# Kernel optimization log

Hardware: AMD Instinct MI355X
Metric: run time of the kernel (lower is better)

## Reference

```python
import jax, jax.numpy as jnp
import numpy as np

D_MODEL = 512
B, T = 4, 4096


def setup_inputs() -> dict:
    key = jax.random.key(0)
    k1, k2, k3 = jax.random.split(key, 3)
    x = jax.random.normal(k1, (B, T, D_MODEL), dtype=jnp.float32)
    # torch nn.Linear weight layout: [out_features, in_features]
    w_qkv = jax.random.normal(k2, (3 * D_MODEL, D_MODEL), dtype=jnp.float32) * (1.0 / np.sqrt(D_MODEL))
    w_proj = jax.random.normal(k3, (D_MODEL, D_MODEL), dtype=jnp.float32) * (1.0 / np.sqrt(D_MODEL))
    return {"x": x, "w_qkv": w_qkv, "w_proj": w_proj}


def reference(x, w_qkv, w_proj):
    # Faithful to the torch module: NO head split; attention over full d_model.
    Bx, Tx, C = x.shape
    qkv = jnp.einsum('btc,oc->bto', x, w_qkv)  # [B,T,3C]
    q, k, v = jnp.split(qkv, 3, axis=-1)
    scale = 1.0 / jnp.sqrt(jnp.asarray(C, x.dtype))
    scores = jnp.einsum('btc,bsc->bts', q, k) * scale  # [B,T,T]
    causal = jnp.tril(jnp.ones((Tx, Tx), dtype=bool))
    scores = jnp.where(causal[None, :, :], scores, -jnp.inf)
    weights = jax.nn.softmax(scores, axis=-1)
    out = jnp.einsum('bts,bsc->btc', weights, v)
    return jnp.einsum('btc,oc->bto', out, w_proj)
```

## Files before the change

kernel.cpp:

```cpp
#include <hip/hip_runtime.h>
#include <hip/hip_bf16.h>
#include <stdint.h>

typedef __bf16 bf16_t;
typedef __bf16 bf16x4 __attribute__((ext_vector_type(4)));
typedef __bf16 bf16x8 __attribute__((ext_vector_type(8)));
typedef short s16x4 __attribute__((ext_vector_type(4)));
typedef float f32x4 __attribute__((ext_vector_type(4)));

static_assert(sizeof(bf16x8) == 16, "bf16x8 must be 16B");

#define MFMA_BF16(a, b, c) __builtin_amdgcn_mfma_f32_16x16x32_bf16((a), (b), (c), 0, 0, 0)

__device__ __forceinline__ f32x4 mfma16(bf16x4 a, bf16x4 b, f32x4 c) {
#if __has_builtin(__builtin_amdgcn_mfma_f32_16x16x16bf16_1k)
  union { bf16x4 h; s16x4 s; } ua, ub;
  ua.h = a;
  ub.h = b;
  return __builtin_amdgcn_mfma_f32_16x16x16bf16_1k(ua.s, ub.s, c, 0, 0, 0);
#else
  f32x4 d = c;
  asm volatile("v_mfma_f32_16x16x16_bf16 %0, %1, %2, %0" : "+v"(d) : "v"(a), "v"(b));
  return d;
#endif
}

typedef const __attribute__((address_space(1))) void* gas_ptr;
typedef __attribute__((address_space(3))) void* las_ptr;

__device__ __forceinline__ void gload_lds16(const void* g, void* l) {
  __builtin_amdgcn_global_load_lds((gas_ptr)g, (las_ptr)l, 16, 0, 0);
}

#define NEG_BIG (-1.0e30f)

__global__ __launch_bounds__(256) void cvt_kernel(const float* __restrict__ src,
                                                  bf16_t* __restrict__ dst) {
  const int i = (blockIdx.x * 256 + threadIdx.x) * 4;
  const f32x4 v = *(const f32x4*)(src + i);
  bf16x4 o;
  o[0] = (bf16_t)v[0];
  o[1] = (bf16_t)v[1];
  o[2] = (bf16_t)v[2];
  o[3] = (bf16_t)v[3];
  *(bf16x4*)(dst + i) = o;
}

template <int MODE>
__global__ __launch_bounds__(256, 2) void gemm_bt_kernel(
    const bf16_t* __restrict__ A, const bf16_t* __restrict__ Bw,
    bf16_t* __restrict__ o_q, bf16_t* __restrict__ o_k, bf16_t* __restrict__ o_vT,
    float* __restrict__ o_f) {
  constexpr int K = 512;
  __shared__ bf16_t As[128 * 32];
  __shared__ bf16_t Bs[128 * 32];

  const int tid = threadIdx.x;
  const int lane = tid & 63;
  const int wid = tid >> 6;
  const int quad = lane >> 4;
  const int l15 = lane & 15;
  const int wm = wid >> 1;
  const int wn = wid & 1;

  const int mt = blockIdx.x & 127;
  const int nt = blockIdx.x >> 7;
  const int row0 = mt * 128;
  const int col0 = nt * 128;

  f32x4 acc[4][4] = {};

  for (int kt = 0; kt < K; kt += 32) {
    __syncthreads();
#pragma unroll
    for (int rnd = 0; rnd < 2; rnd++) {
      const int e = (rnd * 256 + tid) * 8;
      const int r = e >> 5;
      const int c = e & 31;
      gload_lds16(A + (size_t)(row0 + r) * K + kt + c, As + e);
      gload_lds16(Bw + (size_t)(col0 + r) * K + kt + c, Bs + e);
    }
    __syncthreads();

    bf16x8 af[4], bfr[4];
#pragma unroll
    for (int i = 0; i < 4; i++)
      af[i] = *(const bf16x8*)(As + (wm * 64 + i * 16 + l15) * 32 + quad * 8);
#pragma unroll
    for (int i = 0; i < 4; i++)
      bfr[i] = *(const bf16x8*)(Bs + (wn * 64 + i * 16 + l15) * 32 + quad * 8);
#pragma unroll
    for (int mi = 0; mi < 4; mi++)
#pragma unroll
      for (int ni = 0; ni < 4; ni++)
        acc[mi][ni] = MFMA_BF16(af[mi], bfr[ni], acc[mi][ni]);
  }

#pragma unroll
  for (int mi = 0; mi < 4; mi++) {
    const int row = row0 + wm * 64 + mi * 16 + quad * 4;
#pragma unroll
    for (int ni = 0; ni < 4; ni++) {
      const int col = col0 + wn * 64 + ni * 16 + l15;
#pragma unroll
      for (int r = 0; r < 4; r++) {
        const int rr = row + r;
        if constexpr (MODE == 0) {
          const bf16_t bv = (bf16_t)acc[mi][ni][r];
          if (col < 512) {
            o_q[(size_t)rr * 512 + col] = bv;
          } else if (col < 1024) {
            o_k[(size_t)rr * 512 + (col - 512)] = bv;
          } else {
            const int bb = rr >> 12;
            const int t = rr & 4095;
            o_vT[((size_t)bb * 512 + (col - 1024)) * 4096 + t] = bv;
          }
        } else {
          o_f[(size_t)rr * 512 + col] = acc[mi][ni][r];
        }
      }
    }
  }
}

__global__ __launch_bounds__(256, 2) void attn_part_kernel(
    const bf16_t* __restrict__ q, const bf16_t* __restrict__ k,
    const bf16_t* __restrict__ vT, bf16_t* __restrict__ partO,
    float2* __restrict__ stats) {
  __shared__ bf16_t SB[2][16384];

  const int tid = threadIdx.x;
  const int lane = tid & 63;
  const int wid = tid >> 6;
  const int quad = lane >> 4;
  const int l15 = lane & 15;

  const int bid = blockIdx.x;
  const int b = bid & 3;
  const int w = bid >> 2;
  int g = 0;
  while (w >= 4 * (g + 1) * (g + 2)) g++;
  const int rem = w - 4 * g * (g + 1);
  const int i = rem / (g + 1);
  const int c = rem - i * (g + 1);
  const int s = 8 * g + i;

  const int t0w = s * 64 + wid * 16;
  const int kv0 = c * 512;
  const int mmax = min(31, (t0w + 15 - kv0) >> 4);
  const int kvtmax = mmax >> 2;
  const int mmax_blk = min(31, (s * 64 + 63 - kv0) >> 4);
  const int kvtmax_blk = mmax_blk >> 2;

  const float scale = 0.044194173824159216f;
  const bf16_t* kbase = k + ((size_t)b * 4096 + kv0) * 512;
  const bf16_t* vbase = vT + ((size_t)b * 512) * 4096 + kv0;

  auto stageK = [&](int kt, int buf) {
    for (int rnd = 0; rnd <= kvtmax_blk; rnd++) {
      const int ch = rnd * 256 + tid;
      const int g4 = ch >> 4;
      const int w16 = ch & 15;
      const int cg = (w16 >> 2) ^ (g4 & 3);
      const int row = g4 * 4 + (w16 & 3);
      gload_lds16(kbase + (size_t)row * 512 + kt * 32 + cg * 8,
                  &SB[buf][ch * 8]);
    }
  };
  auto stageV = [&](int dh, int kvt, int buf) {
    const bf16_t* vb = vbase + (size_t)(dh * 256) * 4096;
#pragma unroll
    for (int rnd = 0; rnd < 8; rnd++) {
      const int ch = rnd * 256 + tid;
      const int d = ch >> 3;
      const int cg = (ch & 7) ^ (d & 7);
      gload_lds16(vb + (size_t)d * 4096 + kvt * 64 + cg * 8, &SB[buf][ch * 8]);
    }
  };

  stageK(0, 0);

  bf16x8 qf[16];
  {
    const bf16_t* qp = q + ((size_t)(b * 4096 + t0w + l15)) * 512 + quad * 8;
#pragma unroll
    for (int kk = 0; kk < 16; kk++) qf[kk] = *(const bf16x8*)(qp + kk * 32);
  }

  f32x4 Sacc[32];
#pragma unroll
  for (int m = 0; m < 32; m++) Sacc[m] = f32x4{0.f, 0.f, 0.f, 0.f};

  const int abase =
      ((l15 >> 2) * 16 + (quad ^ ((l15 >> 2) & 3)) * 4 + (l15 & 3)) * 8;

  __syncthreads();

  int cur = 0;
#pragma unroll
  for (int kt = 0; kt < 16; kt++) {
    if (kt < 15)
      stageK(kt + 1, cur ^ 1);
    else
      stageV(0, 0, cur ^ 1);

    const bf16_t* sb = &SB[cur][0];
    __builtin_amdgcn_s_setprio(1);
#pragma unroll
    for (int m = 0; m < 32; m++) {
      if (m <= mmax) {
        const bf16x8 kf = *(const bf16x8*)(sb + abase + m * 512);
        Sacc[m] = MFMA_BF16(kf, qf[kt], Sacc[m]);
      }
    }
    __builtin_amdgcn_s_setprio(0);
    __syncthreads();
    cur ^= 1;
  }

  const int qr = t0w + l15;
  float mx = NEG_BIG;
#pragma unroll
  for (int m = 0; m < 32; m++) {
    if (m <= mmax) {
#pragma unroll
      for (int r = 0; r < 4; r++) {
        const int kv = kv0 + m * 16 + quad * 4 + r;
        const float vvv = (kv <= qr) ? Sacc[m][r] : NEG_BIG;
        Sacc[m][r] = vvv;
        mx = fmaxf(mx, vvv);
      }
    }
  }
  mx = fmaxf(mx, __shfl_xor(mx, 16));
  mx = fmaxf(mx, __shfl_xor(mx, 32));

  float lrow = 0.0f;
  bf16x4 pb[32];
#pragma unroll
  for (int m = 0; m < 32; m++) {
    bf16x4 pv = {};
    if (m <= mmax) {
#pragma unroll
      for (int r = 0; r < 4; r++) {
        const float p = __expf((Sacc[m][r] - mx) * scale);
        pv[r] = (bf16_t)p;
        lrow += p;
      }
    }
    pb[m] = pv;
  }
  lrow += __shfl_xor(lrow, 16);
  lrow += __shfl_xor(lrow, 32);

  if (quad == 0)
    stats[((size_t)w * 4 + b) * 64 + wid * 16 + l15] =
        make_float2(mx * scale, lrow);

  const int l64 = l15 * 64;
  const int qh = quad >> 1;
  const int ql = (quad & 1) * 4;
  const int s7 = l15 & 7;

  for (int dh = 0; dh < 2; dh++) {
    f32x4 Oacc[16];
#pragma unroll
    for (int dt = 0; dt < 16; dt++) Oacc[dt] = f32x4{0.f, 0.f, 0.f, 0.f};

    for (int kvt = 0; kvt <= kvtmax_blk; kvt++) {
      if (kvt < kvtmax_blk)
        stageV(dh, kvt + 1, cur ^ 1);
      else if (dh == 0)
        stageV(1, 0, cur ^ 1);

      if (kvt <= kvtmax) {
        const bf16_t* sb = &SB[cur][0];
        __builtin_amdgcn_s_setprio(1);
#pragma unroll
        for (int dt = 0; dt < 16; dt++) {
#pragma unroll
          for (int gg = 0; gg < 4; gg++) {
            const bf16x4 vf = *(const bf16x4*)(
                sb + dt * 1024 + l64 + (((gg * 2 + qh) ^ s7) << 3) + ql);
            Oacc[dt] = mfma16(pb[kvt * 4 + gg], vf, Oacc[dt]);
          }
        }
        __builtin_amdgcn_s_setprio(0);
      }
      __syncthreads();
      cur ^= 1;
    }

    bf16_t* pbase = partO + (size_t)bid * 32768 + dh * 256;
#pragma unroll
    for (int rr = 0; rr < 4; rr++) {
      bf16_t* prow = pbase + (size_t)(wid * 16 + quad * 4 + rr) * 512 + l15;
#pragma unroll
      for (int dt = 0; dt < 16; dt++) prow[dt * 16] = (bf16_t)Oacc[dt][rr];
    }
  }
}

__global__ __launch_bounds__(256) void attn_combine_kernel(
    const bf16_t* __restrict__ partO, const float2* __restrict__ stats,
    bf16_t* __restrict__ o) {
  const int b = blockIdx.x & 3;
  const int s = blockIdx.x >> 2;
  const int g = s >> 3;
  const int nc = g + 1;
  const int w0 = 4 * g * (g + 1) + (s & 7) * (g + 1);

  __shared__ float wgt[8][64];
  __shared__ float linv[64];

  const int tid = threadIdx.x;
  if (tid < 64) {
    float mc[8], lc[8];
    float M = NEG_BIG;
    for (int cc = 0; cc < nc; cc++) {
      const float2 ml = stats[((size_t)(w0 + cc) * 4 + b) * 64 + tid];
      mc[cc] = ml.x;
      lc[cc] = ml.y;
      M = fmaxf(M, ml.x);
    }
    float L = 0.0f;
    for (int cc = 0; cc < nc; cc++) {
      const float wv = __expf(mc[cc] - M);
      wgt[cc][tid] = wv;
      L += wv * lc[cc];
    }
    linv[tid] = (L > 0.0f) ? 1.0f / L : 0.0f;
  }
  __syncthreads();

#pragma unroll
  for (int it = 0; it < 16; it++) {
    const int idx = it * 256 + tid;
    const int row = idx >> 6;
    const int d8 = (idx & 63) * 8;
    float acc[8] = {};
    for (int cc = 0; cc < nc; cc++) {
      const int bidc = ((w0 + cc) << 2) | b;
      const bf16x8 p = *(const bf16x8*)(partO + (size_t)bidc * 32768 +
                                        (size_t)row * 512 + d8);
      const float wv = wgt[cc][row];
#pragma unroll
      for (int e = 0; e < 8; e++) acc[e] += wv * (float)p[e];
    }
    const float li = linv[row];
    bf16x8 ov;
#pragma unroll
    for (int e = 0; e < 8; e++) ov[e] = (bf16_t)(acc[e] * li);
    *(bf16x8*)(o + ((size_t)(b * 4096 + s * 64 + row)) * 512 + d8) = ov;
  }
}

extern "C" void kernel_launch(void* const* d_in, const int* in_sizes, int n_in,
                              void* d_out, int out_size, void* d_ws, size_t ws_size,
                              hipStream_t stream) {
  const float* x_f = (const float*)d_in[0];
  const float* wq_f = (const float*)d_in[1];
  const float* wp_f = (const float*)d_in[2];
  float* out = (float*)d_out;

  bf16_t* xb = (bf16_t*)d_ws;
  bf16_t* wqb = xb + (size_t)16384 * 512;
  bf16_t* wpb = wqb + (size_t)1536 * 512;
  bf16_t* q = wpb + (size_t)512 * 512;
  bf16_t* kk = q + (size_t)16384 * 512;
  bf16_t* vT = kk + (size_t)16384 * 512;
  bf16_t* partO = vT + (size_t)16384 * 512;
  float2* stats = (float2*)(partO + (size_t)1152 * 32768);

  cvt_kernel<<<(16384 * 512) / 1024, 256, 0, stream>>>(x_f, xb);
  cvt_kernel<<<(1536 * 512) / 1024, 256, 0, stream>>>(wq_f, wqb);
  cvt_kernel<<<(512 * 512) / 1024, 256, 0, stream>>>(wp_f, wpb);

  gemm_bt_kernel<0><<<128 * 12, 256, 0, stream>>>(xb, wqb, q, kk, vT, nullptr);
  attn_part_kernel<<<1152, 256, 0, stream>>>(q, kk, vT, partO, stats);
  attn_combine_kernel<<<256, 256, 0, stream>>>(partO, stats, xb);
  gemm_bt_kernel<1><<<128 * 4, 256, 0, stream>>>(xb, wpb, nullptr, nullptr, nullptr, out);
}
```

Before: 422.1 us.

## Deepen attention load pipeline, change partial-O layout, merge conversion kernels

The attention-partial kernel now runs one unified slice stream over K and V tiles. It keeps two global-to-LDS loads in flight, gated by explicit vmcnt waits and raw barriers, where before a single prefetch sat behind __syncthreads. Partial outputs are written as contiguous bf16x4 per lane in a fragment-native layout, and the combine kernel reads that layout and transposes through swizzled LDS into coalesced row stores. The three fp32-to-bf16 conversion launches are merged into one. K staging now always issues 8 rounds even when fewer rows are needed, which adds some load traffic, and the hand-tuned waitcnt logic risks ordering bugs.

```diff
diff --git a/kernel.cpp b/kernel.cpp
--- a/kernel.cpp
+++ b/kernel.cpp
@@ -32,18 +32,32 @@
   __builtin_amdgcn_global_load_lds((gas_ptr)g, (las_ptr)l, 16, 0, 0);
 }
 
+#define ORDER_FENCE() asm volatile("" ::: "memory")
+
 #define NEG_BIG (-1.0e30f)
 
-__global__ __launch_bounds__(256) void cvt_kernel(const float* __restrict__ src,
-                                                  bf16_t* __restrict__ dst) {
+__global__ __launch_bounds__(256) void cvt3_kernel(
+    const float* __restrict__ x, const float* __restrict__ wq,
+    const float* __restrict__ wp, bf16_t* __restrict__ xb,
+    bf16_t* __restrict__ wqb, bf16_t* __restrict__ wpb) {
   const int i = (blockIdx.x * 256 + threadIdx.x) * 4;
-  const f32x4 v = *(const f32x4*)(src + i);
+  const float* src;
+  bf16_t* dst;
+  int off;
+  if (i < 8388608) {
+    src = x; dst = xb; off = 0;
+  } else if (i < 9175040) {
+    src = wq; dst = wqb; off = 8388608;
+  } else {
+    src = wp; dst = wpb; off = 9175040;
+  }
+  const f32x4 v = *(const f32x4*)(src + (i - off));
   bf16x4 o;
   o[0] = (bf16_t)v[0];
   o[1] = (bf16_t)v[1];
   o[2] = (bf16_t)v[2];
   o[3] = (bf16_t)v[3];
-  *(bf16x4*)(dst + i) = o;
+  *(bf16x4*)(dst + (i - off)) = o;
 }
 
 template <int MODE>
@@ -151,35 +165,44 @@
   const int mmax = min(31, (t0w + 15 - kv0) >> 4);
   const int kvtmax = mmax >> 2;
   const int mmax_blk = min(31, (s * 64 + 63 - kv0) >> 4);
-  const int kvtmax_blk = mmax_blk >> 2;
+  const int NV = (mmax_blk >> 2) + 1;
+  const int NSLICE = 16 + 2 * NV;
 
   const float scale = 0.044194173824159216f;
   const bf16_t* kbase = k + ((size_t)b * 4096 + kv0) * 512;
   const bf16_t* vbase = vT + ((size_t)b * 512) * 4096 + kv0;
 
-  auto stageK = [&](int kt, int buf) {
-    for (int rnd = 0; rnd <= kvtmax_blk; rnd++) {
-      const int ch = rnd * 256 + tid;
-      const int g4 = ch >> 4;
-      const int w16 = ch & 15;
-      const int cg = (w16 >> 2) ^ (g4 & 3);
-      const int row = g4 * 4 + (w16 & 3);
-      gload_lds16(kbase + (size_t)row * 512 + kt * 32 + cg * 8,
-                  &SB[buf][ch * 8]);
+  auto stage_slice = [&](int u, int buf) {
+    if (u < 16) {
+#pragma unroll
+      for (int rnd = 0; rnd < 8; rnd++) {
+        const int ch = rnd * 256 + tid;
+        const int g4 = ch >> 4;
+        const int w16 = ch & 15;
+        const int cg = (w16 >> 2) ^ (g4 & 3);
+        const int row = g4 * 4 + (w16 & 3);
+        gload_lds16(kbase + (size_t)row * 512 + u * 32 + cg * 8,
+                    &SB[buf][ch * 8]);
+      }
+    } else {
+      const int v = u - 16;
+      const int dh = (v >= NV) ? 1 : 0;
+      const int kvt = v - dh * NV;
+      const bf16_t* vb = vbase + (size_t)(dh * 256) * 4096;
+#pragma unroll
+      for (int rnd = 0; rnd < 8; rnd++) {
+        const int ch = rnd * 256 + tid;
+        const int d = ch >> 3;
+        const int cg = (ch & 7) ^ (d & 7);
+        gload_lds16(vb + (size_t)d * 4096 + kvt * 64 + cg * 8, &SB[buf][ch * 8]);
+      }
     }
   };
-  auto stageV = [&](int dh, int kvt, int buf) {
-    const bf16_t* vb = vbase + (size_t)(dh * 256) * 4096;
-#pragma unroll
-    for (int rnd = 0; rnd < 8; rnd++) {
-      const int ch = rnd * 256 + tid;
-      const int d = ch >> 3;
-      const int cg = (ch & 7) ^ (d & 7);
-      gload_lds16(vb + (size_t)d * 4096 + kvt * 64 + cg * 8, &SB[buf][ch * 8]);
-    }
-  };
-
-  stageK(0, 0);
+
+  stage_slice(0, 0);
+  ORDER_FENCE();
+  stage_slice(1, 1);
+  ORDER_FENCE();
 
   bf16x8 qf[16];
   {
@@ -195,16 +218,12 @@
   const int abase =
       ((l15 >> 2) * 16 + (quad ^ ((l15 >> 2) & 3)) * 4 + (l15 & 3)) * 8;
 
-  __syncthreads();
-
   int cur = 0;
 #pragma unroll
   for (int kt = 0; kt < 16; kt++) {
-    if (kt < 15)
-      stageK(kt + 1, cur ^ 1);
-    else
-      stageV(0, 0, cur ^ 1);
-
+    asm volatile("s_waitcnt vmcnt(8)" ::: "memory");
+    __builtin_amdgcn_sched_barrier(0);
+    __builtin_amdgcn_s_barrier();
     const bf16_t* sb = &SB[cur][0];
     __builtin_amdgcn_s_setprio(1);
 #pragma unroll
@@ -215,7 +234,10 @@
       }
     }
     __builtin_amdgcn_s_setprio(0);
-    __syncthreads();
+    asm volatile("s_waitcnt lgkmcnt(0)" ::: "memory");
+    __builtin_amdgcn_sched_barrier(0);
+    __builtin_amdgcn_s_barrier();
+    stage_slice(kt + 2, cur);
     cur ^= 1;
   }
 
@@ -263,41 +285,53 @@
   const int ql = (quad & 1) * 4;
   const int s7 = l15 & 7;
 
+#pragma unroll
   for (int dh = 0; dh < 2; dh++) {
     f32x4 Oacc[16];
 #pragma unroll
     for (int dt = 0; dt < 16; dt++) Oacc[dt] = f32x4{0.f, 0.f, 0.f, 0.f};
 
-    for (int kvt = 0; kvt <= kvtmax_blk; kvt++) {
-      if (kvt < kvtmax_blk)
-        stageV(dh, kvt + 1, cur ^ 1);
-      else if (dh == 0)
-        stageV(1, 0, cur ^ 1);
-
-      if (kvt <= kvtmax) {
-        const bf16_t* sb = &SB[cur][0];
-        __builtin_amdgcn_s_setprio(1);
-#pragma unroll
-        for (int dt = 0; dt < 16; dt++) {
-#pragma unroll
-          for (int gg = 0; gg < 4; gg++) {
-            const bf16x4 vf = *(const bf16x4*)(
-                sb + dt * 1024 + l64 + (((gg * 2 + qh) ^ s7) << 3) + ql);
-            Oacc[dt] = mfma16(pb[kvt * 4 + gg], vf, Oacc[dt]);
+#pragma unroll
+    for (int kvt = 0; kvt < 8; kvt++) {
+      if (kvt < NV) {
+        const int u = 16 + dh * NV + kvt;
+        if (u < NSLICE - 1)
+          asm volatile("s_waitcnt vmcnt(8)" ::: "memory");
+        else
+          asm volatile("s_waitcnt vmcnt(0)" ::: "memory");
+        __builtin_amdgcn_sched_barrier(0);
+        __builtin_amdgcn_s_barrier();
+        if (kvt <= kvtmax) {
+          const bf16_t* sb = &SB[cur][0];
+          __builtin_amdgcn_s_setprio(1);
+#pragma unroll
+          for (int dt = 0; dt < 16; dt++) {
+#pragma unroll
+            for (int gg = 0; gg < 4; gg++) {
+              const bf16x4 vf = *(const bf16x4*)(
+                  sb + dt * 1024 + l64 + (((gg * 2 + qh) ^ s7) << 3) + ql);
+              Oacc[dt] = mfma16(pb[kvt * 4 + gg], vf, Oacc[dt]);
+            }
+          }
+          __builtin_amdgcn_s_setprio(0);
+        }
+        if (kvt == NV - 1) {
+          bf16_t* pbase =
+              partO + (size_t)bid * 32768 + dh * 16384 + wid * 4096;
+#pragma unroll
+          for (int dt = 0; dt < 16; dt++) {
+            bf16x4 ov;
+#pragma unroll
+            for (int r = 0; r < 4; r++) ov[r] = (bf16_t)Oacc[dt][r];
+            *(bf16x4*)(pbase + dt * 256 + l15 * 16 + quad * 4) = ov;
           }
         }
-        __builtin_amdgcn_s_setprio(0);
-      }
-      __syncthreads();
-      cur ^= 1;
-    }
-
-    bf16_t* pbase = partO + (size_t)bid * 32768 + dh * 256;
-#pragma unroll
-    for (int rr = 0; rr < 4; rr++) {
-      bf16_t* prow = pbase + (size_t)(wid * 16 + quad * 4 + rr) * 512 + l15;
-#pragma unroll
-      for (int dt = 0; dt < 16; dt++) prow[dt * 16] = (bf16_t)Oacc[dt][rr];
+        asm volatile("s_waitcnt lgkmcnt(0)" ::: "memory");
+        __builtin_amdgcn_sched_barrier(0);
+        __builtin_amdgcn_s_barrier();
+        if (u + 2 < NSLICE) stage_slice(u + 2, cur);
+        cur ^= 1;
+      }
     }
   }
 }
@@ -313,6 +347,7 @@
 
   __shared__ float wgt[8][64];
   __shared__ float linv[64];
+  __shared__ bf16_t TB[64 * 256];
 
   const int tid = threadIdx.x;
   if (tid < 64) {
@@ -334,25 +369,46 @@
   }
   __syncthreads();
 
-#pragma unroll
-  for (int it = 0; it < 16; it++) {
-    const int idx = it * 256 + tid;
-    const int row = idx >> 6;
-    const int d8 = (idx & 63) * 8;
-    float acc[8] = {};
+  const int quad = tid & 3;
+  const int l15 = (tid >> 2) & 15;
+  const int wid = tid >> 6;
+  const int q0 = wid * 16 + quad * 4;
+  const f32x4 li4 = *(const f32x4*)(&linv[q0]);
+
+  for (int dh = 0; dh < 2; dh++) {
+    f32x4 acc4[16] = {};
     for (int cc = 0; cc < nc; cc++) {
-      const int bidc = ((w0 + cc) << 2) | b;
-      const bf16x8 p = *(const bf16x8*)(partO + (size_t)bidc * 32768 +
-                                        (size_t)row * 512 + d8);
-      const float wv = wgt[cc][row];
-#pragma unroll
-      for (int e = 0; e < 8; e++) acc[e] += wv * (float)p[e];
-    }
-    const float li = linv[row];
-    bf16x8 ov;
-#pragma unroll
-    for (int e = 0; e < 8; e++) ov[e] = (bf16_t)(acc[e] * li);
-    *(bf16x8*)(o + ((size_t)(b * 4096 + s * 64 + row)) * 512 + d8) = ov;
+      const bf16_t* pp = partO + (size_t)(((w0 + cc) << 2) | b) * 32768 +
+                         dh * 16384 + wid * 4096 + l15 * 16 + quad * 4;
+      const f32x4 wv4 = *(const f32x4*)(&wgt[cc][q0]);
+#pragma unroll
+      for (int dt = 0; dt < 16; dt++) {
+        const bf16x4 p = *(const bf16x4*)(pp + dt * 256);
+#pragma unroll
+        for (int e = 0; e < 4; e++) acc4[dt][e] += wv4[e] * (float)p[e];
+      }
+    }
+#pragma unroll
+    for (int dt = 0; dt < 16; dt++) {
+      const int d2 = (dt * 16 + l15) * 2;
+#pragma unroll
+      for (int r = 0; r < 4; r++) {
+        const int qq = q0 + r;
+        *(bf16_t*)((char*)TB + qq * 512 + (d2 ^ ((qq & 7) << 4))) =
+            (bf16_t)(acc4[dt][r] * li4[r]);
+      }
+    }
+    __syncthreads();
+    const int row = tid >> 2;
+    const int quarter = tid & 3;
+    bf16_t* orow =
+        o + ((size_t)(b * 4096 + s * 64 + row)) * 512 + dh * 256 + quarter * 64;
+#pragma unroll
+    for (int j = 0; j < 8; j++) {
+      const int byte = row * 512 + ((quarter * 128 + j * 16) ^ ((row & 7) << 4));
+      *(bf16x8*)(orow + j * 8) = *(const bf16x8*)((const char*)TB + byte);
+    }
+    __syncthreads();
   }
 }
 
@@ -373,9 +429,7 @@
   bf16_t* partO = vT + (size_t)16384 * 512;
   float2* stats = (float2*)(partO + (size_t)1152 * 32768);
 
-  cvt_kernel<<<(16384 * 512) / 1024, 256, 0, stream>>>(x_f, xb);
-  cvt_kernel<<<(1536 * 512) / 1024, 256, 0, stream>>>(wq_f, wqb);
-  cvt_kernel<<<(512 * 512) / 1024, 256, 0, stream>>>(wp_f, wpb);
+  cvt3_kernel<<<9216, 256, 0, stream>>>(x_f, wq_f, wp_f, xb, wqb, wpb);
 
   gemm_bt_kernel<0><<<128 * 12, 256, 0, stream>>>(xb, wqb, q, kk, vT, nullptr);
   attn_part_kernel<<<1152, 256, 0, stream>>>(q, kk, vT, partO, stats);
```

Result: slower. 435.5 us (+3.2%).
